# Optimization experiments

Measured on AMD Instinct MI355X. Metric: run time of the kernel, lower is better.

## Reference

```python
import jax, jax.numpy as jnp
import numpy as np

B, C, H, W = 1, 448, 64, 64
K, M, PAD, STRIDE = 7, 7, 3, 1
CG = C // K          # key/query channels (KeyQueryMap divides by k) = 64
GP_HID = int(0.5 * CG)  # geometry prior hidden channels = 32
K2 = K * K
CENTER = K2 // 2


def conv1x1(x, w, b):
    # x: (B, Cin, H, W), w: (Cout, Cin), b: (Cout,)
    return jnp.einsum('bchw,oc->bohw', x, w) + b[None, :, None, None]


def unfold(x):
    # torch.nn.Unfold(K, dilation=1, padding=PAD, stride=STRIDE)
    # output layout: (B, Cin*K2, L) with dim1 index = c*K2 + (di*K + dj)
    Bc, Cc, Hc, Wc = x.shape
    xp = jnp.pad(x, ((0, 0), (0, 0), (PAD, PAD), (PAD, PAD)))
    Ho = (Hc + 2 * PAD - K) // STRIDE + 1
    Wo = (Wc + 2 * PAD - K) // STRIDE + 1
    patches = [xp[:, :, di:di + Ho * STRIDE:STRIDE, dj:dj + Wo * STRIDE:STRIDE]
               for di in range(K) for dj in range(K)]
    u = jnp.stack(patches, axis=2)  # (B, Cc, K2, Ho, Wo)
    return u.reshape(Bc, Cc * K2, Ho * Wo), Ho, Wo


def geometry_prior(gp_w1, gp_b1, gp_w2, gp_b2):
    ar = jnp.arange(-(K // 2), K // 2 + 1, dtype=jnp.float32)   # -3..3
    x_pos = jnp.broadcast_to(ar[None, :], (K, K))
    y_pos = jnp.broadcast_to(ar[::-1][:, None], (K, K))          # 3..-3 down rows
    pos = jnp.stack([x_pos, y_pos], axis=0)[None]                # (1, 2, K, K)
    h = jax.nn.relu(conv1x1(pos, gp_w1, gp_b1))
    out = conv1x1(h, gp_w2, gp_b2)                               # (1, CG, K, K)
    return out.reshape(1, CG, 1, K2)


def setup_inputs() -> dict:
    key = jax.random.key(0)
    ks = jax.random.split(key, 12)
    def lin(k, cout, cin):
        return jax.random.normal(k, (cout, cin), jnp.float32) / np.sqrt(cin)
    inp = {
        'x': jax.random.normal(ks[0], (B, C, H, W), jnp.float32),
        'Wk': lin(ks[1], CG, C), 'bk': jnp.zeros((CG,), jnp.float32),
        'Wq': lin(ks[2], CG, C), 'bq': jnp.zeros((CG,), jnp.float32),
        'gp_w1': lin(ks[3], GP_HID, 2), 'gp_b1': jax.random.normal(ks[4], (GP_HID,), jnp.float32) * 0.01,
        'gp_w2': lin(ks[5], CG, GP_HID), 'gp_b2': jax.random.normal(ks[6], (CG,), jnp.float32) * 0.01,
        'Wf': lin(ks[7], C, C), 'bf': jnp.zeros((C,), jnp.float32),
    }
    return inp


def reference(x, Wk, bk, Wq, bq, gp_w1, gp_b1, gp_w2, gp_b2, Wf, bf):
    gpk = geometry_prior(gp_w1, gp_b1, gp_w2, gp_b2)        # (1, CG, 1, K2)
    km = conv1x1(x, Wk, bk)                                  # (B, CG, H, W)
    qm = conv1x1(x, Wq, bq)
    ku, Ho, Wo = unfold(km)
    L = Ho * Wo
    ku = ku.reshape(B, CG, L, K2)   # same row-major semantics as torch .view
    qu, _, _ = unfold(qm)
    qu = qu.reshape(B, CG, L, K2)
    ak = ku * qu[:, :, :, CENTER:CENTER + 1]                 # (B, CG, L, K2)
    ck = jax.nn.softmax(ak + gpk, axis=-1)                   # (B, CG, L, K2)
    xu, _, _ = unfold(x)
    xu = xu.reshape(B, M, C // M, L, K2)                     # (B, M, CG, L, K2)
    # ck broadcasts over the M axis (valid since B == 1); sum over window dim
    pre = jnp.einsum('bglp,bmglp->bmgl', ck, xu).reshape(B, C, Ho, Wo)
    return conv1x1(pre, Wf, bf)
```

## Files before the change

kernel.cpp:

```cpp
#include <hip/hip_runtime.h>
#include <hip/hip_bf16.h>

#define CC   448
#define CGC  64
#define MMM  7
#define HWSZ 4096
#define KK2  49
#define GPH  32

typedef __attribute__((ext_vector_type(8))) short   short8;
typedef __attribute__((ext_vector_type(4))) float   f32x4;
typedef __attribute__((ext_vector_type(4))) unsigned short us4;

__device__ __forceinline__ unsigned short f2b(float f) {
    union { __hip_bfloat16 h; unsigned short u; } cv;
    cv.h = __float2bfloat16(f);
    return cv.u;
}

__device__ __forceinline__ void mfma_gemm64(
    const float* __restrict__ A,
    const float* __restrict__ B,
    const float* __restrict__ bias,
    float* __restrict__ C,
    int nT, int tid)
{
    __shared__ unsigned short As[2048];
    __shared__ unsigned short Bs[2048];
    __shared__ float bias_s[64];
    if (tid < 64) bias_s[tid] = bias[tid];

    const int lane = tid & 63;
    const int wid  = tid >> 6;
    const int wm   = (wid >> 1) * 32;
    const int wn   = (wid & 1) * 32;
    const int l15  = lane & 15;
    const int l4   = lane >> 4;

    f32x4 acc[2][2];
    #pragma unroll
    for (int i = 0; i < 2; ++i)
        #pragma unroll
        for (int j = 0; j < 2; ++j)
            acc[i][j] = (f32x4){0.f, 0.f, 0.f, 0.f};

    for (int kt = 0; kt < 14; ++kt) {
        #pragma unroll
        for (int it = 0; it < 2; ++it) {
            int ee = tid + it * 256;
            int m = ee >> 3, k4 = ee & 7;
            float4 v = *(const float4*)(A + m * CC + kt * 32 + k4 * 4);
            us4 w = { f2b(v.x), f2b(v.y), f2b(v.z), f2b(v.w) };
            *(us4*)&As[(k4 >> 1) * 512 + m * 8 + (k4 & 1) * 4] = w;
        }
        #pragma unroll
        for (int it = 0; it < 2; ++it) {
            int ee = tid + it * 256;
            int k = ee >> 4, n4 = ee & 15;
            float4 v = *(const float4*)(B + (size_t)(kt * 32 + k) * HWSZ + nT + n4 * 4);
            int base = (k >> 3) * 512 + n4 * 32 + (k & 7);
            Bs[base]      = f2b(v.x);
            Bs[base + 8]  = f2b(v.y);
            Bs[base + 16] = f2b(v.z);
            Bs[base + 24] = f2b(v.w);
        }
        __syncthreads();
        short8 a0 = *(short8*)&As[l4 * 512 + (wm + l15) * 8];
        short8 a1 = *(short8*)&As[l4 * 512 + (wm + 16 + l15) * 8];
        short8 b0 = *(short8*)&Bs[l4 * 512 + (wn + l15) * 8];
        short8 b1 = *(short8*)&Bs[l4 * 512 + (wn + 16 + l15) * 8];
        acc[0][0] = __builtin_amdgcn_mfma_f32_16x16x32_bf16(a0, b0, acc[0][0], 0, 0, 0);
        acc[0][1] = __builtin_amdgcn_mfma_f32_16x16x32_bf16(a0, b1, acc[0][1], 0, 0, 0);
        acc[1][0] = __builtin_amdgcn_mfma_f32_16x16x32_bf16(a1, b0, acc[1][0], 0, 0, 0);
        acc[1][1] = __builtin_amdgcn_mfma_f32_16x16x32_bf16(a1, b1, acc[1][1], 0, 0, 0);
        __syncthreads();
    }
    #pragma unroll
    for (int wm2 = 0; wm2 < 2; ++wm2)
        #pragma unroll
        for (int wn2 = 0; wn2 < 2; ++wn2)
            #pragma unroll
            for (int r = 0; r < 4; ++r) {
                int row = wm + wm2 * 16 + l4 * 4 + r;
                int col = wn + wn2 * 16 + l15;
                C[(size_t)row * HWSZ + nT + col] = acc[wm2][wn2][r] + bias_s[row];
            }
}

__global__ __launch_bounds__(256) void kq_mfma(
    const float* __restrict__ x,
    const float* __restrict__ Wk, const float* __restrict__ bk,
    const float* __restrict__ Wq, const float* __restrict__ bq,
    float* __restrict__ km, float* __restrict__ qm)
{
    const bool isQ = (blockIdx.y != 0);
    mfma_gemm64(isQ ? Wq : Wk, x, isQ ? bq : bk, isQ ? qm : km,
                blockIdx.x * 64, threadIdx.x);
}

__global__ __launch_bounds__(256) void fconv_mfma(
    const float* __restrict__ pre,
    const float* __restrict__ Wf, const float* __restrict__ bfv,
    float* __restrict__ out)
{
    const int mt = blockIdx.y;
    mfma_gemm64(Wf + (size_t)mt * 64 * CC, pre, bfv + mt * 64,
                out + (size_t)mt * 64 * HWSZ, blockIdx.x * 64, threadIdx.x);
}

#define GLO 196
#define GHI 260
#define XWORDS (GLO + HWSZ + GHI)

__device__ __forceinline__ int win_off_global(int n, bool& ok) {
    int p  = n >> 12;
    int l  = n & 4095;
    int di = (p * 37) >> 8;
    int dj = p - di * 7;
    int i  = (l >> 6) + di - 3;
    int j  = (l & 63) + dj - 3;
    ok = ((unsigned)i < 64u) && ((unsigned)j < 64u);
    return i * 64 + j;
}

__global__ __launch_bounds__(512) void attn_kernel(
    const float* __restrict__ km, const float* __restrict__ qm,
    const float* __restrict__ x,
    const float* __restrict__ gw1, const float* __restrict__ gb1,
    const float* __restrict__ gw2, const float* __restrict__ gb2,
    float* __restrict__ pre)
{
    __shared__ float klin[XWORDS];
    __shared__ float xlin[XWORDS];
    __shared__ float gpk_s[KK2];
    const int tid = threadIdx.x;
    const int g   = blockIdx.y;
    const int lp  = blockIdx.x * 512 + tid;

    if (tid < 114) {
        float4 z = {0.f, 0.f, 0.f, 0.f};
        int w = (tid < 49) ? tid * 4 : (GLO + HWSZ + (tid - 49) * 4);
        *(float4*)&klin[w] = z;
        *(float4*)&xlin[w] = z;
    }
    {
        const float4* km4 = (const float4*)(km + (size_t)g * HWSZ);
        float4 va = km4[tid], vb = km4[tid + 512];
        *(float4*)&klin[GLO + tid * 4]         = va;
        *(float4*)&klin[GLO + (tid + 512) * 4] = vb;
    }
    if (tid < KK2) {
        int di = tid / 7, dj = tid - di * 7;
        float xp = (float)(dj - 3);
        float yp = (float)(3 - di);
        float acc = gb2[g];
        #pragma unroll
        for (int j = 0; j < GPH; ++j) {
            float h = gw1[j * 2 + 0] * xp + gw1[j * 2 + 1] * yp + gb1[j];
            h = fmaxf(h, 0.f);
            acc = fmaf(gw2[g * GPH + j], h, acc);
        }
        gpk_s[tid] = acc;
    }

    float qc;
    { bool ok; int o = win_off_global(lp * KK2 + 24, ok); qc = ok ? qm[(size_t)g * HWSZ + o] : 0.f; }

    const int n0 = lp * KK2;
    const int p0 = n0 >> 12;
    const int l0 = n0 & 4095;
    const int ts = ((p0 + 1) << 12) - n0;
    const int di0 = (p0 * 37) >> 8, dj0 = p0 - di0 * 7;
    const int p1  = p0 + 1;
    const int di1 = (p1 * 37) >> 8, dj1 = p1 - di1 * 7;
    const int djm3_0 = dj0 - 3, djm3_1 = dj1 - 3;
    const int B0 = GLO + l0 + (di0 - 3) * 64 + djm3_0;
    const int B1 = GLO + l0 - 4096 + (di1 - 3) * 64 + djm3_1;
    __syncthreads();

    float a[KK2];
    float mx = -1e30f;
    #pragma unroll
    for (int t = 0; t < KK2; ++t) {
        bool s1 = (t >= ts);
        int base = s1 ? B1 : B0;
        float kv = klin[base + t];
        int jj = ((l0 + t) & 63) + (s1 ? djm3_1 : djm3_0);
        kv = ((unsigned)jj < 64u) ? kv : 0.f;
        float av = fmaf(kv, qc, gpk_s[t]);
        a[t] = av;
        mx = fmaxf(mx, av);
    }
    float d = 0.f;
    #pragma unroll
    for (int t = 0; t < KK2; ++t) {
        float e = __expf(a[t] - mx);
        d += e;
        bool s1 = (t >= ts);
        int jj = ((l0 + t) & 63) + (s1 ? djm3_1 : djm3_0);
        a[t] = ((unsigned)jj < 64u) ? e : 0.f;
    }
    const float inv = 1.f / d;

    for (int m = 0; m < MMM; ++m) {
        const float4* xg4 = (const float4*)(x + (size_t)(m * CGC + g) * HWSZ);
        float4 va = xg4[tid], vb = xg4[tid + 512];
        __syncthreads();
        *(float4*)&xlin[GLO + tid * 4]         = va;
        *(float4*)&xlin[GLO + (tid + 512) * 4] = vb;
        __syncthreads();
        float acc = 0.f;
        #pragma unroll
        for (int t = 0; t < KK2; ++t) {
            int base = (t >= ts) ? B1 : B0;
            acc = fmaf(a[t], xlin[base + t], acc);
        }
        pre[(size_t)(m * CGC + g) * HWSZ + lp] = acc * inv;
    }
}

extern "C" void kernel_launch(void* const* d_in, const int* in_sizes, int n_in,
                              void* d_out, int out_size, void* d_ws, size_t ws_size,
                              hipStream_t stream) {
    const float* x   = (const float*)d_in[0];
    const float* Wk  = (const float*)d_in[1];
    const float* bk  = (const float*)d_in[2];
    const float* Wq  = (const float*)d_in[3];
    const float* bq  = (const float*)d_in[4];
    const float* gw1 = (const float*)d_in[5];
    const float* gb1 = (const float*)d_in[6];
    const float* gw2 = (const float*)d_in[7];
    const float* gb2 = (const float*)d_in[8];
    const float* Wf  = (const float*)d_in[9];
    const float* bfv = (const float*)d_in[10];
    float* out = (float*)d_out;

    float* km  = (float*)d_ws;
    float* qm  = km + CGC * HWSZ;
    float* pre = qm + CGC * HWSZ;

    kq_mfma   <<<dim3(64, 2),   256, 0, stream>>>(x, Wk, bk, Wq, bq, km, qm);
    attn_kernel<<<dim3(8, CGC), 512, 0, stream>>>(km, qm, x, gw1, gb1, gw2, gb2, pre);
    fconv_mfma<<<dim3(64, 7),   256, 0, stream>>>(pre, Wf, bfv, out);
}
```

Measured before the change: 133.3 us.

## Register-prefetch next tiles in MFMA GEMMs and attention; halve attention block size

The shared bf16 GEMM now loads the next K-slice of A and B into registers while the current slice is written to LDS and consumed by MFMAs, so global latency overlaps compute. The attention kernel shrinks blocks to 256 threads (doubling the grid) and prefetches the next x channel slab into registers before the LDS store/sync of the current one. The cost is extra register pressure, and each attention block now loads the full km/x planes for half as many outputs, doubling that staging traffic.

```diff
diff --git a/kernel.cpp b/kernel.cpp
--- a/kernel.cpp
+++ b/kernel.cpp
@@ -37,6 +37,11 @@
     const int l15  = lane & 15;
     const int l4   = lane >> 4;
 
+    const int am0 = tid >> 3,          ak0 = tid & 7;
+    const int am1 = (tid + 256) >> 3,  ak1 = (tid + 256) & 7;
+    const int bk0 = tid >> 4,          bn0 = tid & 15;
+    const int bk1 = (tid + 256) >> 4,  bn1 = (tid + 256) & 15;
+
     f32x4 acc[2][2];
     #pragma unroll
     for (int i = 0; i < 2; ++i)
@@ -44,35 +49,44 @@
         for (int j = 0; j < 2; ++j)
             acc[i][j] = (f32x4){0.f, 0.f, 0.f, 0.f};
 
+    float4 a0 = *(const float4*)(A + am0 * CC + ak0 * 4);
+    float4 a1 = *(const float4*)(A + am1 * CC + ak1 * 4);
+    float4 b0 = *(const float4*)(B + (size_t)bk0 * HWSZ + nT + bn0 * 4);
+    float4 b1 = *(const float4*)(B + (size_t)bk1 * HWSZ + nT + bn1 * 4);
+
     for (int kt = 0; kt < 14; ++kt) {
-        #pragma unroll
-        for (int it = 0; it < 2; ++it) {
-            int ee = tid + it * 256;
-            int m = ee >> 3, k4 = ee & 7;
-            float4 v = *(const float4*)(A + m * CC + kt * 32 + k4 * 4);
-            us4 w = { f2b(v.x), f2b(v.y), f2b(v.z), f2b(v.w) };
-            *(us4*)&As[(k4 >> 1) * 512 + m * 8 + (k4 & 1) * 4] = w;
-        }
-        #pragma unroll
-        for (int it = 0; it < 2; ++it) {
-            int ee = tid + it * 256;
-            int k = ee >> 4, n4 = ee & 15;
-            float4 v = *(const float4*)(B + (size_t)(kt * 32 + k) * HWSZ + nT + n4 * 4);
-            int base = (k >> 3) * 512 + n4 * 32 + (k & 7);
-            Bs[base]      = f2b(v.x);
-            Bs[base + 8]  = f2b(v.y);
-            Bs[base + 16] = f2b(v.z);
-            Bs[base + 24] = f2b(v.w);
-        }
-        __syncthreads();
-        short8 a0 = *(short8*)&As[l4 * 512 + (wm + l15) * 8];
-        short8 a1 = *(short8*)&As[l4 * 512 + (wm + 16 + l15) * 8];
-        short8 b0 = *(short8*)&Bs[l4 * 512 + (wn + l15) * 8];
-        short8 b1 = *(short8*)&Bs[l4 * 512 + (wn + 16 + l15) * 8];
-        acc[0][0] = __builtin_amdgcn_mfma_f32_16x16x32_bf16(a0, b0, acc[0][0], 0, 0, 0);
-        acc[0][1] = __builtin_amdgcn_mfma_f32_16x16x32_bf16(a0, b1, acc[0][1], 0, 0, 0);
-        acc[1][0] = __builtin_amdgcn_mfma_f32_16x16x32_bf16(a1, b0, acc[1][0], 0, 0, 0);
-        acc[1][1] = __builtin_amdgcn_mfma_f32_16x16x32_bf16(a1, b1, acc[1][1], 0, 0, 0);
+        {
+            us4 w0 = { f2b(a0.x), f2b(a0.y), f2b(a0.z), f2b(a0.w) };
+            *(us4*)&As[(ak0 >> 1) * 512 + am0 * 8 + (ak0 & 1) * 4] = w0;
+            us4 w1 = { f2b(a1.x), f2b(a1.y), f2b(a1.z), f2b(a1.w) };
+            *(us4*)&As[(ak1 >> 1) * 512 + am1 * 8 + (ak1 & 1) * 4] = w1;
+            int base0 = (bk0 >> 3) * 512 + bn0 * 32 + (bk0 & 7);
+            Bs[base0]      = f2b(b0.x);
+            Bs[base0 + 8]  = f2b(b0.y);
+            Bs[base0 + 16] = f2b(b0.z);
+            Bs[base0 + 24] = f2b(b0.w);
+            int base1 = (bk1 >> 3) * 512 + bn1 * 32 + (bk1 & 7);
+            Bs[base1]      = f2b(b1.x);
+            Bs[base1 + 8]  = f2b(b1.y);
+            Bs[base1 + 16] = f2b(b1.z);
+            Bs[base1 + 24] = f2b(b1.w);
+        }
+        if (kt < 13) {
+            int ko = (kt + 1) * 32;
+            a0 = *(const float4*)(A + am0 * CC + ko + ak0 * 4);
+            a1 = *(const float4*)(A + am1 * CC + ko + ak1 * 4);
+            b0 = *(const float4*)(B + (size_t)(ko + bk0) * HWSZ + nT + bn0 * 4);
+            b1 = *(const float4*)(B + (size_t)(ko + bk1) * HWSZ + nT + bn1 * 4);
+        }
+        __syncthreads();
+        short8 fa0 = *(short8*)&As[l4 * 512 + (wm + l15) * 8];
+        short8 fa1 = *(short8*)&As[l4 * 512 + (wm + 16 + l15) * 8];
+        short8 fb0 = *(short8*)&Bs[l4 * 512 + (wn + l15) * 8];
+        short8 fb1 = *(short8*)&Bs[l4 * 512 + (wn + 16 + l15) * 8];
+        acc[0][0] = __builtin_amdgcn_mfma_f32_16x16x32_bf16(fa0, fb0, acc[0][0], 0, 0, 0);
+        acc[0][1] = __builtin_amdgcn_mfma_f32_16x16x32_bf16(fa0, fb1, acc[0][1], 0, 0, 0);
+        acc[1][0] = __builtin_amdgcn_mfma_f32_16x16x32_bf16(fa1, fb0, acc[1][0], 0, 0, 0);
+        acc[1][1] = __builtin_amdgcn_mfma_f32_16x16x32_bf16(fa1, fb1, acc[1][1], 0, 0, 0);
         __syncthreads();
     }
     #pragma unroll
@@ -123,7 +137,7 @@
     return i * 64 + j;
 }
 
-__global__ __launch_bounds__(512) void attn_kernel(
+__global__ __launch_bounds__(256) void attn_kernel(
     const float* __restrict__ km, const float* __restrict__ qm,
     const float* __restrict__ x,
     const float* __restrict__ gw1, const float* __restrict__ gb1,
@@ -135,7 +149,7 @@
     __shared__ float gpk_s[KK2];
     const int tid = threadIdx.x;
     const int g   = blockIdx.y;
-    const int lp  = blockIdx.x * 512 + tid;
+    const int lp  = blockIdx.x * 256 + tid;
 
     if (tid < 114) {
         float4 z = {0.f, 0.f, 0.f, 0.f};
@@ -145,9 +159,11 @@
     }
     {
         const float4* km4 = (const float4*)(km + (size_t)g * HWSZ);
-        float4 va = km4[tid], vb = km4[tid + 512];
-        *(float4*)&klin[GLO + tid * 4]         = va;
-        *(float4*)&klin[GLO + (tid + 512) * 4] = vb;
+        #pragma unroll
+        for (int i = 0; i < 4; ++i) {
+            int idx = tid + i * 256;
+            *(float4*)&klin[GLO + idx * 4] = km4[idx];
+        }
     }
     if (tid < KK2) {
         int di = tid / 7, dj = tid - di * 7;
@@ -176,6 +192,12 @@
     const int djm3_0 = dj0 - 3, djm3_1 = dj1 - 3;
     const int B0 = GLO + l0 + (di0 - 3) * 64 + djm3_0;
     const int B1 = GLO + l0 - 4096 + (di1 - 3) * 64 + djm3_1;
+
+    float4 xr0, xr1, xr2, xr3;
+    {
+        const float4* xg4 = (const float4*)(x + (size_t)g * HWSZ);
+        xr0 = xg4[tid]; xr1 = xg4[tid + 256]; xr2 = xg4[tid + 512]; xr3 = xg4[tid + 768];
+    }
     __syncthreads();
 
     float a[KK2];
@@ -202,12 +224,17 @@
     }
     const float inv = 1.f / d;
 
+    #pragma unroll 1
     for (int m = 0; m < MMM; ++m) {
-        const float4* xg4 = (const float4*)(x + (size_t)(m * CGC + g) * HWSZ);
-        float4 va = xg4[tid], vb = xg4[tid + 512];
-        __syncthreads();
-        *(float4*)&xlin[GLO + tid * 4]         = va;
-        *(float4*)&xlin[GLO + (tid + 512) * 4] = vb;
+        __syncthreads();
+        *(float4*)&xlin[GLO + tid * 4]          = xr0;
+        *(float4*)&xlin[GLO + (tid + 256) * 4]  = xr1;
+        *(float4*)&xlin[GLO + (tid + 512) * 4]  = xr2;
+        *(float4*)&xlin[GLO + (tid + 768) * 4]  = xr3;
+        if (m < MMM - 1) {
+            const float4* xg4 = (const float4*)(x + (size_t)((m + 1) * CGC + g) * HWSZ);
+            xr0 = xg4[tid]; xr1 = xg4[tid + 256]; xr2 = xg4[tid + 512]; xr3 = xg4[tid + 768];
+        }
         __syncthreads();
         float acc = 0.f;
         #pragma unroll
@@ -239,7 +266,7 @@
     float* qm  = km + CGC * HWSZ;
     float* pre = qm + CGC * HWSZ;
 
-    kq_mfma   <<<dim3(64, 2),   256, 0, stream>>>(x, Wk, bk, Wq, bq, km, qm);
-    attn_kernel<<<dim3(8, CGC), 512, 0, stream>>>(km, qm, x, gw1, gb1, gw2, gb2, pre);
-    fconv_mfma<<<dim3(64, 7),   256, 0, stream>>>(pre, Wf, bfv, out);
-}
+    kq_mfma    <<<dim3(64, 2),  256, 0, stream>>>(x, Wk, bk, Wq, bq, km, qm);
+    attn_kernel<<<dim3(16, CGC), 256, 0, stream>>>(km, qm, x, gw1, gb1, gw2, gb2, pre);
+    fconv_mfma <<<dim3(64, 7),  256, 0, stream>>>(pre, Wf, bfv, out);
+}
```

Measured after the change: 118.8 us. -10.8%, faster.
